# Optimization experiments

Hardware: AMD Instinct MI355X
Metric: run time of the kernel (lower is better)

## Reference

```python
import jax, jax.numpy as jnp
import numpy as np
from jax import lax

WINDOW_SIZE = 11
SIGMA = 1.5
CHANNEL = 1
DATA_RANGE = 1.0
C1 = (0.01 * DATA_RANGE) ** 2
C2 = (0.03 * DATA_RANGE) ** 2


def _gaussian_window(size, sigma, channel):
    coords = jnp.arange(size, dtype=jnp.float32) - size // 2
    g = jnp.exp(-coords ** 2 / (2.0 * sigma ** 2))
    g = g / g.sum()
    w2d = g[:, None] * g[None, :]                    # (size, size)
    # depthwise weight layout OIHW: (channel, 1, size, size)
    return jnp.broadcast_to(w2d[None, None], (channel, 1, size, size))


def setup_inputs() -> dict:
    key = jax.random.key(0)
    k1, k2 = jax.random.split(key)
    B, C, H, W = 64, CHANNEL, 512, 512
    x = jax.random.uniform(k1, (B, C, H, W), dtype=jnp.float32)
    y = jax.random.uniform(k2, (B, C, H, W), dtype=jnp.float32)
    window = _gaussian_window(WINDOW_SIZE, SIGMA, CHANNEL)
    return {"x": x, "y": y, "window": window}


def _apply_window(t, window):
    pad = WINDOW_SIZE // 2
    return lax.conv_general_dilated(
        t, window,
        window_strides=(1, 1),
        padding=((pad, pad), (pad, pad)),
        dimension_numbers=("NCHW", "OIHW", "NCHW"),
        feature_group_count=CHANNEL,
    )


def reference(x, y, window):
    mu_x = _apply_window(x, window)
    mu_y = _apply_window(y, window)
    mu_x_sq = mu_x ** 2
    mu_y_sq = mu_y ** 2
    mu_xy = mu_x * mu_y
    sigma_x_sq = _apply_window(x * x, window) - mu_x_sq
    sigma_y_sq = _apply_window(y * y, window) - mu_y_sq
    sigma_xy = _apply_window(x * y, window) - mu_xy
    numerator = (2.0 * mu_xy + C1) * (2.0 * sigma_xy + C2)
    denominator = (mu_x_sq + mu_y_sq + C1) * (sigma_x_sq + sigma_y_sq + C2)
    ssim_map = numerator / denominator
    ssim_per_sample = ssim_map.mean(axis=(1, 2, 3))
    return ssim_per_sample.mean()  # reduction='mean'
```

## Files before the change

kernel.cpp:

```cpp
#include <hip/hip_runtime.h>


#define IMG 512
#define TW 64
#define TH 32
#define SAB 78
#define NTHREADS 320

typedef __attribute__((ext_vector_type(2))) float f32x2;

static __device__ __forceinline__ f32x2 pk_fma(f32x2 a, f32x2 b, f32x2 c) {
    f32x2 d;
    asm("v_pk_fma_f32 %0, %1, %2, %3" : "=v"(d) : "v"(a), "v"(b), "v"(c));
    return d;
}
static __device__ __forceinline__ f32x2 pk_mul(f32x2 a, f32x2 b) {
    f32x2 d;
    asm("v_pk_mul_f32 %0, %1, %2" : "=v"(d) : "v"(a), "v"(b));
    return d;
}

__global__ __launch_bounds__(NTHREADS, 5) void ssim_fused(
    const float* __restrict__ x, const float* __restrict__ y,
    const float* __restrict__ win, float* __restrict__ partial)
{
    __shared__ __align__(16) f32x2 vab[TH][SAB];
    __shared__ __align__(16) f32x2 vqq[TH][SAB];
    __shared__ float sg[11];
    __shared__ float redbuf[5];

    const int tid = threadIdx.x;

    if (tid < 11) {
        float s = 0.f;
        #pragma unroll
        for (int j = 0; j < 11; ++j) s += win[tid * 11 + j];
        sg[tid] = s;
    }

    const int x0 = blockIdx.x * TW;
    const int y0 = blockIdx.y * TH;
    const size_t img_off = (size_t)blockIdx.z * (IMG * IMG);
    const float* __restrict__ xb = x + img_off;
    const float* __restrict__ yb = y + img_off;

    const int sgm = tid / 80;
    const int c   = tid - sgm * 80;
    const int r0  = sgm * 8;
    const int gx  = x0 + c - 5;
    const int cw  = (c < 76) ? c : 75;

    const bool cok = (gx >= 0) && (gx < IMG);
    f32x2 pab[18];
    #pragma unroll
    for (int j = 0; j < 18; ++j) {
        int gy = y0 + r0 - 5 + j;
        bool ok = cok && (gy >= 0) && (gy < IMG);
        int o = ok ? (gy * IMG + gx) : 0;
        float a = xb[o];
        float b = yb[o];
        a = ok ? a : 0.f;
        b = ok ? b : 0.f;
        pab[j][0] = a + b;
        pab[j][1] = a - b;
    }

    __syncthreads();
    f32x2 g2[11];
    #pragma unroll
    for (int k = 0; k < 11; ++k) { float gv = sg[k]; g2[k][0] = gv; g2[k][1] = gv; }

    {
        f32x2 t[18];
        #pragma unroll
        for (int j = 0; j < 18; ++j) t[j] = pk_mul(pab[j], pab[j]);
        #pragma unroll
        for (int i = 0; i < 8; ++i) {
            f32x2 q = (f32x2)(0.f);
            #pragma unroll
            for (int k = 0; k < 11; ++k) q = pk_fma(g2[k], t[i + k], q);
            vqq[r0 + i][cw] = q;
        }
    }
    {
        #pragma unroll
        for (int i = 0; i < 8; ++i) {
            f32x2 a = (f32x2)(0.f);
            #pragma unroll
            for (int k = 0; k < 11; ++k) a = pk_fma(g2[k], pab[i + k], a);
            vab[r0 + i][cw] = a;
        }
    }

    __syncthreads();

    const float C1 = 1.0e-4f;
    const float C2 = 9.0e-4f;
    float acc = 0.f;

    if (tid < 256) {
        const int rr = tid >> 3;
        const int c0 = (tid & 7) * 8;

        f32x2 mu[8], qq[8];
        {
            f32x2 t[18];
            const float4* p = (const float4*)&vab[rr][c0];
            #pragma unroll
            for (int q = 0; q < 9; ++q) {
                float4 f = p[q];
                t[2*q][0] = f.x;  t[2*q][1] = f.y;
                t[2*q+1][0] = f.z;  t[2*q+1][1] = f.w;
            }
            #pragma unroll
            for (int i = 0; i < 8; ++i) {
                f32x2 a = (f32x2)(0.f);
                #pragma unroll
                for (int k = 0; k < 11; ++k) a = pk_fma(g2[k], t[i + k], a);
                mu[i] = a;
            }
        }
        {
            f32x2 t[18];
            const float4* p = (const float4*)&vqq[rr][c0];
            #pragma unroll
            for (int q = 0; q < 9; ++q) {
                float4 f = p[q];
                t[2*q][0] = f.x;  t[2*q][1] = f.y;
                t[2*q+1][0] = f.z;  t[2*q+1][1] = f.w;
            }
            #pragma unroll
            for (int i = 0; i < 8; ++i) {
                f32x2 a = (f32x2)(0.f);
                #pragma unroll
                for (int k = 0; k < 11; ++k) a = pk_fma(g2[k], t[i + k], a);
                qq[i] = a;
            }
        }

        #pragma unroll
        for (int i = 0; i < 8; ++i) {
            f32x2 m2 = pk_mul(mu[i], mu[i]);
            float P = m2[0] + m2[1];
            float Q = m2[0] - m2[1];
            float R = qq[i][0] + qq[i][1];
            float S = qq[i][0] - qq[i][1];
            float num1 = fmaf(0.5f, Q, C1);
            float num2 = fmaf(0.5f, S - Q, C2);
            float den1 = fmaf(0.5f, P, C1);
            float den2 = fmaf(0.5f, R - P, C2);
            acc += (num1 * num2) * __builtin_amdgcn_rcpf(den1 * den2);
        }
    }

    #pragma unroll
    for (int off = 32; off > 0; off >>= 1) acc += __shfl_down(acc, off, 64);
    int wid = tid >> 6, lane = tid & 63;
    if (lane == 0) redbuf[wid] = acc;
    __syncthreads();
    if (tid == 0) {
        float ssum = redbuf[0] + redbuf[1] + redbuf[2] + redbuf[3] + redbuf[4];
        partial[((size_t)blockIdx.z * gridDim.y + blockIdx.y) * gridDim.x + blockIdx.x] = ssum;
    }
}

#define NPART 8192

__global__ __launch_bounds__(1024) void ssim_finalize(
    const float* __restrict__ partial, float* __restrict__ out)
{
    __shared__ double red[16];
    double acc = 0.0;
    #pragma unroll
    for (int q = 0; q < NPART / 1024; ++q) acc += (double)partial[q * 1024 + threadIdx.x];
    #pragma unroll
    for (int off = 32; off > 0; off >>= 1) acc += __shfl_down(acc, off, 64);
    int wid = threadIdx.x >> 6, lane = threadIdx.x & 63;
    if (lane == 0) red[wid] = acc;
    __syncthreads();
    if (threadIdx.x == 0) {
        double ssum = 0.0;
        #pragma unroll
        for (int w = 0; w < 16; ++w) ssum += red[w];
        out[0] = (float)(ssum / (64.0 * 512.0 * 512.0));
    }
}

extern "C" void kernel_launch(void* const* d_in, const int* in_sizes, int n_in,
                              void* d_out, int out_size, void* d_ws, size_t ws_size,
                              hipStream_t stream) {
    (void)in_sizes; (void)n_in; (void)out_size; (void)ws_size;
    const float* x   = (const float*)d_in[0];
    const float* y   = (const float*)d_in[1];
    const float* win = (const float*)d_in[2];
    float* out = (float*)d_out;
    float* partial = (float*)d_ws;

    dim3 grid(IMG / TW, IMG / TH, 64);
    ssim_fused<<<grid, NTHREADS, 0, stream>>>(x, y, win, partial);
    ssim_finalize<<<1, 1024, 0, stream>>>(partial, out);
}
```

Before: 181.6 us.

## Switch to full-width row bands with a rolling vertical window over chunks

Each block now handles a full-width band of 64 rows. It slides an 18-row register window down the band in 8-row chunks, so the vertical halo is loaded once per band instead of once per 32-row tile, and there is no horizontal halo reload because the whole width is covered. Shared memory holds one 8-row chunk with zero-padded borders, and two barriers per chunk separate the vertical and horizontal passes. The grid shrinks to 512 blocks of 512 threads, which lowers parallelism and adds a serial chunk loop with syncs, but cuts redundant halo loads and finalize work.

```diff
diff --git a/kernel.cpp b/kernel.cpp
--- a/kernel.cpp
+++ b/kernel.cpp
@@ -2,10 +2,11 @@
 
 
 #define IMG 512
-#define TW 64
-#define TH 32
-#define SAB 78
-#define NTHREADS 320
+#define BH 64
+#define CHUNK 8
+#define NCHUNK (BH / CHUNK)
+#define SROW 524
+#define NTHREADS 512
 
 typedef __attribute__((ext_vector_type(2))) float f32x2;
 
@@ -20,14 +21,14 @@
     return d;
 }
 
-__global__ __launch_bounds__(NTHREADS, 5) void ssim_fused(
+__global__ __launch_bounds__(NTHREADS, 4) void ssim_band(
     const float* __restrict__ x, const float* __restrict__ y,
     const float* __restrict__ win, float* __restrict__ partial)
 {
-    __shared__ __align__(16) f32x2 vab[TH][SAB];
-    __shared__ __align__(16) f32x2 vqq[TH][SAB];
+    __shared__ __align__(16) f32x2 vab[CHUNK][SROW];
+    __shared__ __align__(16) f32x2 vqq[CHUNK][SROW];
     __shared__ float sg[11];
-    __shared__ float redbuf[5];
+    __shared__ float redbuf[NTHREADS / 64];
 
     const int tid = threadIdx.x;
 
@@ -37,30 +38,24 @@
         for (int j = 0; j < 11; ++j) s += win[tid * 11 + j];
         sg[tid] = s;
     }
-
-    const int x0 = blockIdx.x * TW;
-    const int y0 = blockIdx.y * TH;
-    const size_t img_off = (size_t)blockIdx.z * (IMG * IMG);
-    const float* __restrict__ xb = x + img_off;
-    const float* __restrict__ yb = y + img_off;
-
-    const int sgm = tid / 80;
-    const int c   = tid - sgm * 80;
-    const int r0  = sgm * 8;
-    const int gx  = x0 + c - 5;
-    const int cw  = (c < 76) ? c : 75;
-
-    const bool cok = (gx >= 0) && (gx < IMG);
+    if (tid < 160) {
+        int plane = tid / 80, rem = tid % 80, row = rem / 10, pc = rem % 10;
+        int cc = (pc < 5) ? pc : (512 + pc);
+        f32x2 z = (f32x2)(0.f);
+        if (plane == 0) vab[row][cc] = z; else vqq[row][cc] = z;
+    }
+
+    const int y0 = blockIdx.x * BH;
+    const size_t img_off = (size_t)blockIdx.y * (IMG * IMG);
+    const float* __restrict__ xb = x + img_off + tid;
+    const float* __restrict__ yb = y + img_off + tid;
+
     f32x2 pab[18];
     #pragma unroll
-    for (int j = 0; j < 18; ++j) {
-        int gy = y0 + r0 - 5 + j;
-        bool ok = cok && (gy >= 0) && (gy < IMG);
-        int o = ok ? (gy * IMG + gx) : 0;
-        float a = xb[o];
-        float b = yb[o];
-        a = ok ? a : 0.f;
-        b = ok ? b : 0.f;
+    for (int j = 0; j < 10; ++j) {
+        int gy = y0 - 5 + j;
+        float a = 0.f, b = 0.f;
+        if (gy >= 0) { a = xb[gy * IMG]; b = yb[gy * IMG]; }
         pab[j][0] = a + b;
         pab[j][1] = a - b;
     }
@@ -69,88 +64,100 @@
     f32x2 g2[11];
     #pragma unroll
     for (int k = 0; k < 11; ++k) { float gv = sg[k]; g2[k][0] = gv; g2[k][1] = gv; }
-
-    {
-        f32x2 t[18];
-        #pragma unroll
-        for (int j = 0; j < 18; ++j) t[j] = pk_mul(pab[j], pab[j]);
-        #pragma unroll
-        for (int i = 0; i < 8; ++i) {
-            f32x2 q = (f32x2)(0.f);
-            #pragma unroll
-            for (int k = 0; k < 11; ++k) q = pk_fma(g2[k], t[i + k], q);
-            vqq[r0 + i][cw] = q;
-        }
-    }
-    {
-        #pragma unroll
-        for (int i = 0; i < 8; ++i) {
-            f32x2 a = (f32x2)(0.f);
-            #pragma unroll
-            for (int k = 0; k < 11; ++k) a = pk_fma(g2[k], pab[i + k], a);
-            vab[r0 + i][cw] = a;
-        }
-    }
-
-    __syncthreads();
 
     const float C1 = 1.0e-4f;
     const float C2 = 9.0e-4f;
     float acc = 0.f;
 
-    if (tid < 256) {
-        const int rr = tid >> 3;
-        const int c0 = (tid & 7) * 8;
-
-        f32x2 mu[8], qq[8];
+    const int rr = tid >> 6;
+    const int c0 = (tid & 63) * 8;
+
+    for (int k = 0; k < NCHUNK; ++k) {
+        const int r0 = y0 + k * CHUNK;
+
+        #pragma unroll
+        for (int j = 0; j < 8; ++j) {
+            int gy = r0 + 5 + j;
+            float a = 0.f, b = 0.f;
+            if (gy < IMG) { a = xb[gy * IMG]; b = yb[gy * IMG]; }
+            pab[10 + j][0] = a + b;
+            pab[10 + j][1] = a - b;
+        }
+
+        f32x2 sq[18];
+        #pragma unroll
+        for (int j = 0; j < 18; ++j) sq[j] = pk_mul(pab[j], pab[j]);
+
+        #pragma unroll
+        for (int i = 0; i < CHUNK; ++i) {
+            f32x2 a = (f32x2)(0.f), q = (f32x2)(0.f);
+            #pragma unroll
+            for (int t = 0; t < 11; ++t) {
+                a = pk_fma(g2[t], pab[i + t], a);
+                q = pk_fma(g2[t], sq[i + t], q);
+            }
+            vab[i][tid + 5] = a;
+            vqq[i][tid + 5] = q;
+        }
+
+        __syncthreads();
+
         {
-            f32x2 t[18];
-            const float4* p = (const float4*)&vab[rr][c0];
-            #pragma unroll
-            for (int q = 0; q < 9; ++q) {
-                float4 f = p[q];
-                t[2*q][0] = f.x;  t[2*q][1] = f.y;
-                t[2*q+1][0] = f.z;  t[2*q+1][1] = f.w;
-            }
+            f32x2 mu[8], qq[8];
+            {
+                f32x2 t[18];
+                const float4* p = (const float4*)&vab[rr][c0];
+                #pragma unroll
+                for (int q8 = 0; q8 < 9; ++q8) {
+                    float4 f = p[q8];
+                    t[2*q8][0] = f.x;  t[2*q8][1] = f.y;
+                    t[2*q8+1][0] = f.z;  t[2*q8+1][1] = f.w;
+                }
+                #pragma unroll
+                for (int i = 0; i < 8; ++i) {
+                    f32x2 a = (f32x2)(0.f);
+                    #pragma unroll
+                    for (int t1 = 0; t1 < 11; ++t1) a = pk_fma(g2[t1], t[i + t1], a);
+                    mu[i] = a;
+                }
+            }
+            {
+                f32x2 t[18];
+                const float4* p = (const float4*)&vqq[rr][c0];
+                #pragma unroll
+                for (int q8 = 0; q8 < 9; ++q8) {
+                    float4 f = p[q8];
+                    t[2*q8][0] = f.x;  t[2*q8][1] = f.y;
+                    t[2*q8+1][0] = f.z;  t[2*q8+1][1] = f.w;
+                }
+                #pragma unroll
+                for (int i = 0; i < 8; ++i) {
+                    f32x2 a = (f32x2)(0.f);
+                    #pragma unroll
+                    for (int t1 = 0; t1 < 11; ++t1) a = pk_fma(g2[t1], t[i + t1], a);
+                    qq[i] = a;
+                }
+            }
+
             #pragma unroll
             for (int i = 0; i < 8; ++i) {
-                f32x2 a = (f32x2)(0.f);
-                #pragma unroll
-                for (int k = 0; k < 11; ++k) a = pk_fma(g2[k], t[i + k], a);
-                mu[i] = a;
+                f32x2 m2 = pk_mul(mu[i], mu[i]);
+                float P = m2[0] + m2[1];
+                float Q = m2[0] - m2[1];
+                float R = qq[i][0] + qq[i][1];
+                float S = qq[i][0] - qq[i][1];
+                float num1 = fmaf(0.5f, Q, C1);
+                float num2 = fmaf(0.5f, S - Q, C2);
+                float den1 = fmaf(0.5f, P, C1);
+                float den2 = fmaf(0.5f, R - P, C2);
+                acc += (num1 * num2) * __builtin_amdgcn_rcpf(den1 * den2);
             }
         }
-        {
-            f32x2 t[18];
-            const float4* p = (const float4*)&vqq[rr][c0];
-            #pragma unroll
-            for (int q = 0; q < 9; ++q) {
-                float4 f = p[q];
-                t[2*q][0] = f.x;  t[2*q][1] = f.y;
-                t[2*q+1][0] = f.z;  t[2*q+1][1] = f.w;
-            }
-            #pragma unroll
-            for (int i = 0; i < 8; ++i) {
-                f32x2 a = (f32x2)(0.f);
-                #pragma unroll
-                for (int k = 0; k < 11; ++k) a = pk_fma(g2[k], t[i + k], a);
-                qq[i] = a;
-            }
-        }
-
-        #pragma unroll
-        for (int i = 0; i < 8; ++i) {
-            f32x2 m2 = pk_mul(mu[i], mu[i]);
-            float P = m2[0] + m2[1];
-            float Q = m2[0] - m2[1];
-            float R = qq[i][0] + qq[i][1];
-            float S = qq[i][0] - qq[i][1];
-            float num1 = fmaf(0.5f, Q, C1);
-            float num2 = fmaf(0.5f, S - Q, C2);
-            float den1 = fmaf(0.5f, P, C1);
-            float den2 = fmaf(0.5f, R - P, C2);
-            acc += (num1 * num2) * __builtin_amdgcn_rcpf(den1 * den2);
-        }
+
+        __syncthreads();
+
+        #pragma unroll
+        for (int j = 0; j < 10; ++j) pab[j] = pab[j + 8];
     }
 
     #pragma unroll
@@ -159,20 +166,20 @@
     if (lane == 0) redbuf[wid] = acc;
     __syncthreads();
     if (tid == 0) {
-        float ssum = redbuf[0] + redbuf[1] + redbuf[2] + redbuf[3] + redbuf[4];
-        partial[((size_t)blockIdx.z * gridDim.y + blockIdx.y) * gridDim.x + blockIdx.x] = ssum;
-    }
-}
-
-#define NPART 8192
-
-__global__ __launch_bounds__(1024) void ssim_finalize(
+        float ssum = 0.f;
+        #pragma unroll
+        for (int w = 0; w < NTHREADS / 64; ++w) ssum += redbuf[w];
+        partial[blockIdx.y * gridDim.x + blockIdx.x] = ssum;
+    }
+}
+
+#define NPART 512
+
+__global__ __launch_bounds__(512) void ssim_finalize(
     const float* __restrict__ partial, float* __restrict__ out)
 {
-    __shared__ double red[16];
-    double acc = 0.0;
-    #pragma unroll
-    for (int q = 0; q < NPART / 1024; ++q) acc += (double)partial[q * 1024 + threadIdx.x];
+    __shared__ double red[8];
+    double acc = (double)partial[threadIdx.x];
     #pragma unroll
     for (int off = 32; off > 0; off >>= 1) acc += __shfl_down(acc, off, 64);
     int wid = threadIdx.x >> 6, lane = threadIdx.x & 63;
@@ -181,7 +188,7 @@
     if (threadIdx.x == 0) {
         double ssum = 0.0;
         #pragma unroll
-        for (int w = 0; w < 16; ++w) ssum += red[w];
+        for (int w = 0; w < 8; ++w) ssum += red[w];
         out[0] = (float)(ssum / (64.0 * 512.0 * 512.0));
     }
 }
@@ -196,7 +203,7 @@
     float* out = (float*)d_out;
     float* partial = (float*)d_ws;
 
-    dim3 grid(IMG / TW, IMG / TH, 64);
-    ssim_fused<<<grid, NTHREADS, 0, stream>>>(x, y, win, partial);
-    ssim_finalize<<<1, 1024, 0, stream>>>(partial, out);
-}
+    dim3 grid(IMG / BH, 64);
+    ssim_band<<<grid, NTHREADS, 0, stream>>>(x, y, win, partial);
+    ssim_finalize<<<1, NPART, 0, stream>>>(partial, out);
+}
```

Result: faster. 167.2 us (-7.9%).
